# Kernel optimization log

Measured on AMD Instinct MI355X. Metric: run time of the kernel, lower is better.

The kernel has to match this reference:

```python
import jax, jax.numpy as jnp
import numpy as np

DIM, CTX_DIM, HEADS, HIDDEN = 1024, 768, 16, 4096
HEAD_DIM = DIM // HEADS
SCALE = HEAD_DIM ** -0.5


def _layernorm(x, w, b, eps=1e-5):
    mu = jnp.mean(x, axis=-1, keepdims=True)
    var = jnp.var(x, axis=-1, keepdims=True)
    return (x - mu) * jax.lax.rsqrt(var + eps) * w + b


def _heads(t):  # [B, L, H*D] -> [B, H, L, D]
    B, L, _ = t.shape
    return t.reshape(B, L, HEADS, HEAD_DIM).transpose(0, 2, 1, 3)


def _merge(t):  # [B, H, L, D] -> [B, L, H*D]
    B, H, L, D = t.shape
    return t.transpose(0, 2, 1, 3).reshape(B, L, H * D)


def _attn(xq, xkv, qw, qb, kw, kb, vw, vb, pw, pb):
    q = _heads(xq @ qw.T + qb)
    k = _heads(xkv @ kw.T + kb)
    v = _heads(xkv @ vw.T + vb)
    scores = jnp.einsum('bhld,bhsd->bhls', q, k) * SCALE
    probs = jax.nn.softmax(scores, axis=-1)
    out = _merge(jnp.einsum('bhls,bhsd->bhld', probs, v))
    return out @ pw.T + pb


def setup_inputs() -> dict:
    key = jax.random.key(0)
    ks = jax.random.split(key, 16)
    s = 0.02
    d = {
        'x': jax.random.normal(ks[0], (4, 2048, DIM), jnp.float32),
        'context': jax.random.normal(ks[1], (4, 77, CTX_DIM), jnp.float32),
        'ln1_w': jnp.ones((DIM,)), 'ln1_b': jnp.zeros((DIM,)),
        'ln2_w': jnp.ones((DIM,)), 'ln2_b': jnp.zeros((DIM,)),
        'ln3_w': jnp.ones((DIM,)), 'ln3_b': jnp.zeros((DIM,)),
        'sa_qw': jax.random.normal(ks[2], (DIM, DIM)) * s, 'sa_qb': jnp.zeros((DIM,)),
        'sa_kw': jax.random.normal(ks[3], (DIM, DIM)) * s, 'sa_kb': jnp.zeros((DIM,)),
        'sa_vw': jax.random.normal(ks[4], (DIM, DIM)) * s, 'sa_vb': jnp.zeros((DIM,)),
        'sa_pw': jax.random.normal(ks[5], (DIM, DIM)) * s, 'sa_pb': jnp.zeros((DIM,)),
        'ca_qw': jax.random.normal(ks[6], (DIM, DIM)) * s, 'ca_qb': jnp.zeros((DIM,)),
        'ca_kw': jax.random.normal(ks[7], (DIM, CTX_DIM)) * s, 'ca_kb': jnp.zeros((DIM,)),
        'ca_vw': jax.random.normal(ks[8], (DIM, CTX_DIM)) * s, 'ca_vb': jnp.zeros((DIM,)),
        'ca_pw': jax.random.normal(ks[9], (DIM, DIM)) * s, 'ca_pb': jnp.zeros((DIM,)),
        'fc1_w': jax.random.normal(ks[10], (HIDDEN, DIM)) * s, 'fc1_b': jnp.zeros((HIDDEN,)),
        'fc2_w': jax.random.normal(ks[11], (DIM, HIDDEN)) * s, 'fc2_b': jnp.zeros((DIM,)),
    }
    return d


def reference(x, context, ln1_w, ln1_b, ln2_w, ln2_b, ln3_w, ln3_b,
              sa_qw, sa_qb, sa_kw, sa_kb, sa_vw, sa_vb, sa_pw, sa_pb,
              ca_qw, ca_qb, ca_kw, ca_kb, ca_vw, ca_vb, ca_pw, ca_pb,
              fc1_w, fc1_b, fc2_w, fc2_b):
    h = _layernorm(x, ln1_w, ln1_b)
    x = x + _attn(h, h, sa_qw, sa_qb, sa_kw, sa_kb, sa_vw, sa_vb, sa_pw, sa_pb)
    h = _layernorm(x, ln2_w, ln2_b)
    x = x + _attn(h, context, ca_qw, ca_qb, ca_kw, ca_kb, ca_vw, ca_vb, ca_pw, ca_pb)
    h = _layernorm(x, ln3_w, ln3_b)
    h = jax.nn.gelu(h @ fc1_w.T + fc1_b, approximate=False)  # torch nn.GELU = exact
    x = x + (h @ fc2_w.T + fc2_b)
    return x
```

## Files before the change

### kernel.cpp

```cpp
#include <hip/hip_runtime.h>
#include <hip/hip_bf16.h>
#include <cstdint>
#include <cstddef>

typedef __attribute__((ext_vector_type(8))) short bf16x8;
typedef __attribute__((ext_vector_type(4))) float f32x4;
typedef __attribute__((ext_vector_type(16))) float f32x16;

__device__ __forceinline__ unsigned short f2bf(float f) {
  union { float f; unsigned u; } c; c.f = f;
  unsigned r = c.u + 0x7FFFu + ((c.u >> 16) & 1u);
  return (unsigned short)(r >> 16);
}

__device__ __forceinline__ unsigned cvtpk(float lo, float hi) {
  unsigned r;
  asm("v_cvt_pk_bf16_f32 %0, %1, %2" : "=v"(r) : "v"(lo), "v"(hi));
  return r;
}

__device__ __forceinline__ int xcd_swz(int bid, int nwg) {
  const int cpx = nwg >> 3;
  return (bid & 7) * cpx + (bid >> 3);
}

typedef const __attribute__((address_space(1))) unsigned int* gas_ptr;
typedef __attribute__((address_space(3))) unsigned int* las_ptr;

__device__ __forceinline__ void gload16(const unsigned short* g, unsigned short* l) {
  __builtin_amdgcn_global_load_lds((gas_ptr)g, (las_ptr)l, 16, 0, 0);
}

struct WJ { const float* s; unsigned short* d; int nblk; };
struct WJobs { WJ j[10]; };

__global__ void wconv_k(WJobs jb) {
  const int bid = blockIdx.x;
  int base = 0, ji = -1;
  #pragma unroll
  for (int k = 0; k < 10; ++k) {
    const int nb = jb.j[k].nblk;
    if (ji < 0) { if (bid < base + nb) ji = k; else base += nb; }
  }
  const int i = (bid - base) * 256 + threadIdx.x;
  float4 v = ((const float4*)jb.j[ji].s)[i];
  ushort4 o;
  o.x = f2bf(v.x); o.y = f2bf(v.y); o.z = f2bf(v.z); o.w = f2bf(v.w);
  ((ushort4*)jb.j[ji].d)[i] = o;
}

__global__ void ctxpad_k(const float* __restrict__ ctx, unsigned short* __restrict__ out) {
  int i = blockIdx.x * blockDim.x + threadIdx.x;
  if (i >= 512 * 192) return;
  int r = i / 192, c4 = i % 192;
  int b = r >> 7, s = r & 127;
  ushort4 o = {0, 0, 0, 0};
  if (s < 77) {
    float4 v = ((const float4*)(ctx + (size_t)(b * 77 + s) * 768))[c4];
    o.x = f2bf(v.x); o.y = f2bf(v.y); o.z = f2bf(v.z); o.w = f2bf(v.w);
  }
  ((ushort4*)out)[i] = o;
}

__global__ __launch_bounds__(256)
void ln_k(const float* __restrict__ x, const float* __restrict__ w,
          const float* __restrict__ b, unsigned short* __restrict__ out) {
  int row = blockIdx.x, tid = threadIdx.x;
  float4 v = ((const float4*)(x + (size_t)row * 1024))[tid];
  float s = v.x + v.y + v.z + v.w;
  float s2 = v.x * v.x + v.y * v.y + v.z * v.z + v.w * v.w;
  #pragma unroll
  for (int m = 1; m < 64; m <<= 1) { s += __shfl_xor(s, m); s2 += __shfl_xor(s2, m); }
  __shared__ float ps[4], ps2[4];
  int wv = tid >> 6;
  if ((tid & 63) == 0) { ps[wv] = s; ps2[wv] = s2; }
  __syncthreads();
  s = ps[0] + ps[1] + ps[2] + ps[3];
  s2 = ps2[0] + ps2[1] + ps2[2] + ps2[3];
  float mu = s * (1.0f / 1024.0f);
  float var = s2 * (1.0f / 1024.0f) - mu * mu;
  float rstd = rsqrtf(var + 1e-5f);
  float4 wv4 = ((const float4*)w)[tid];
  float4 bv4 = ((const float4*)b)[tid];
  ushort4 o;
  o.x = f2bf((v.x - mu) * rstd * wv4.x + bv4.x);
  o.y = f2bf((v.y - mu) * rstd * wv4.y + bv4.y);
  o.z = f2bf((v.z - mu) * rstd * wv4.z + bv4.z);
  o.w = f2bf((v.w - mu) * rstd * wv4.w + bv4.w);
  ((ushort4*)(out + (size_t)row * 1024))[tid] = o;
}

#define SG_A(BUF, H, TE)                                                       \
  _Pragma("unroll")                                                            \
  for (int j = 0; j < AHL; ++j)                                                \
    __builtin_amdgcn_global_load_lds(                                          \
        (gas_ptr)(gA + (TE) + (size_t)((H) * (BM / 2) + j * 64) * (size_t)K),  \
        (las_ptr)(lds_all + (BUF) * AELEMS +                                   \
                  (((H) * (BM / 2) + j * 64) + w * 8) * 64),                   \
        16, 0, 0);

#define SG_B(BUF, H, TE)                                                       \
  _Pragma("unroll")                                                            \
  for (int j = 0; j < BHL; ++j)                                                \
    __builtin_amdgcn_global_load_lds(                                          \
        (gas_ptr)(gB + (TE) + (size_t)((H) * (BN / 2) + j * 64) * (size_t)K),  \
        (las_ptr)(lds_all + 2 * AELEMS + (BUF) * BELEMS +                      \
                  (((H) * (BN / 2) + j * 64) + w * 8) * 64),                   \
        16, 0, 0);

#define RD_A(MHh, BUF)                                                         \
  _Pragma("unroll")                                                            \
  for (int i = 0; i < MH; ++i) {                                               \
    const int r = ((MHh) * MH + i) * 32 + wr * 16 + ln;                        \
    _Pragma("unroll")                                                          \
    for (int kc = 0; kc < 2; ++kc)                                             \
      af[i][kc] = *(const bf16x8*)((const char*)lds_all + (BUF) * ABYTES +     \
                    r * 128 + (((kc * 4 + lg) ^ (r & 7)) * 16));               \
  }

#define RD_B(NHh, BUF)                                                         \
  _Pragma("unroll")                                                            \
  for (int i = 0; i < NIH; ++i) {                                              \
    const int ni = (NHh) * NIH + i;                                            \
    const int r = ni * 64 + wcc * 16 + ln;                                     \
    _Pragma("unroll")                                                          \
    for (int kc = 0; kc < 2; ++kc)                                             \
      bfr[ni][kc] = *(const bf16x8*)((const char*)lds_all + 2 * ABYTES +       \
                    (BUF) * BBYTES + r * 128 + (((kc * 4 + lg) ^ (r & 7)) * 16)); \
  }

#define QUAD(MHh, NHh)                                                         \
  __builtin_amdgcn_s_setprio(1);                                               \
  _Pragma("unroll")                                                            \
  for (int kc = 0; kc < 2; ++kc)                                               \
    _Pragma("unroll")                                                          \
    for (int i = 0; i < MH; ++i)                                               \
      _Pragma("unroll")                                                        \
      for (int j2 = 0; j2 < NIH; ++j2) {                                       \
        const int mi = (MHh) * MH + i, ni = (NHh) * NIH + j2;                  \
        if constexpr (SWAP)                                                    \
          acc[mi][ni] = __builtin_amdgcn_mfma_f32_16x16x32_bf16(               \
              bfr[ni][kc], af[i][kc], acc[mi][ni], 0, 0, 0);                   \
        else                                                                   \
          acc[mi][ni] = __builtin_amdgcn_mfma_f32_16x16x32_bf16(               \
              af[i][kc], bfr[ni][kc], acc[mi][ni], 0, 0, 0);                   \
      }                                                                        \
  __builtin_amdgcn_s_setprio(0);

#define VM_TILE()                                                              \
  do { if constexpr (BM == 256) asm volatile("s_waitcnt vmcnt(6)" ::: "memory"); \
       else                     asm volatile("s_waitcnt vmcnt(3)" ::: "memory"); } while (0)

#define TILE(BUF, TE)                                                          \
  {                                                                            \
    const int t = t2 + ((TE) / 64);                                            \
                       \
    RD_A(0, BUF) RD_B(0, BUF)                                                  \
    if (t + 1 < NT) { SG_B((BUF) ^ 1, 1, (TE) + 64) }                          \
    __builtin_amdgcn_s_barrier();                                              \
    asm volatile("s_waitcnt lgkmcnt(0)" ::: "memory");                         \
    __builtin_amdgcn_sched_barrier(0);                                         \
    QUAD(0, 0)                                                                 \
    __builtin_amdgcn_s_barrier();                                              \
                    \
    RD_B(1, BUF)                                                               \
    if (t + 2 < NT) { SG_A(BUF, 0, (TE) + 128) }                               \
    __builtin_amdgcn_s_barrier();                                              \
    asm volatile("s_waitcnt lgkmcnt(0)" ::: "memory");                         \
    __builtin_amdgcn_sched_barrier(0);                                         \
    QUAD(0, 1)                                                                 \
    __builtin_amdgcn_s_barrier();                                              \
                    \
    RD_A(1, BUF)                                                               \
    if (t + 2 < NT) { SG_B(BUF, 0, (TE) + 128) }                               \
    __builtin_amdgcn_s_barrier();                                              \
    asm volatile("s_waitcnt lgkmcnt(0)" ::: "memory");                         \
    __builtin_amdgcn_sched_barrier(0);                                         \
    QUAD(1, 0)                                                                 \
    __builtin_amdgcn_s_barrier();                                              \
     \
    if (t + 2 < NT) { SG_A(BUF, 1, (TE) + 128) }                               \
    __builtin_amdgcn_s_barrier();                                              \
    __builtin_amdgcn_sched_barrier(0);                                         \
    QUAD(1, 1)                                                                 \
    if (t + 2 < NT) { VM_TILE(); }                                             \
    else            { asm volatile("s_waitcnt vmcnt(0)" ::: "memory"); }       \
    __builtin_amdgcn_s_barrier();                                              \
  }

template<int BM, int BN, int EPI, int SWAP, int MINW>
__global__ __launch_bounds__(512, MINW)
void gemm8(const unsigned short* __restrict__ A, const unsigned short* __restrict__ Bw,
           const float* __restrict__ bias0, const float* __restrict__ bias1,
           const float* __restrict__ res, void* __restrict__ C0, void* __restrict__ C1,
           int M, int N, int K, float scale0, int nsplit, int vtL) {
  (void)M;
  constexpr int MI = BM / 32;
  constexpr int MH = MI / 2;
  constexpr int AHL = BM / 128;
  constexpr int NI = BN / 64;
  constexpr int NIH = NI / 2;
  constexpr int BHL = BN / 128;
  constexpr int AELEMS = BM * 64;
  constexpr int BELEMS = BN * 64;
  constexpr int ABYTES = AELEMS * 2;
  constexpr int BBYTES = BELEMS * 2;
  __shared__ unsigned short lds_all[2 * AELEMS + 2 * BELEMS];

  const int tid = threadIdx.x;
  const int w = tid >> 6, lane = tid & 63;
  const int wr = w >> 2, wcc = w & 3;
  const int ln = lane & 15, lg = lane >> 4;
  const int nbn = N / BN;
  const int bid = xcd_swz(blockIdx.x, gridDim.x);
  const int bm = bid / nbn, bn = bid % nbn;
  const int NT = K >> 6;

  const int crow = tid >> 3;
  const int cslot = (tid & 7) ^ (crow & 7);

  const unsigned short* gA = A + ((size_t)(bm * BM) + crow) * K + cslot * 8;
  const unsigned short* gB = Bw + ((size_t)(bn * BN) + crow) * K + cslot * 8;

  bf16x8 af[MH][2], bfr[NI][2];
  f32x4 acc[MI][NI] = {};

  SG_A(0, 0, 0) SG_B(0, 0, 0) SG_B(0, 1, 0) SG_A(0, 1, 0)
  if (NT > 1) { SG_A(1, 0, 64) SG_B(1, 0, 64) SG_A(1, 1, 64) }
  VM_TILE();
  __builtin_amdgcn_s_barrier();

  for (int t2 = 0; t2 < NT; t2 += 2) {
    TILE(0, 0)
    TILE(1, 64)
    gA += 128; gB += 128;
  }

  const int rowbase = bm * BM + wr * 16;
  const int colbase = bn * BN + wcc * 16;
  if constexpr (EPI == 1) {
    #pragma unroll
    for (int ni = 0; ni < NI; ++ni) {
      const int col = colbase + ni * 64 + ln;
      const float bv = bias0[col];
      const int hh = col >> 6, dd = col & 63;
      #pragma unroll
      for (int mi = 0; mi < MI; ++mi) {
        const int row0 = rowbase + mi * 32 + lg * 4;
        const int bb = row0 / vtL, ss = row0 % vtL;
        ushort4 pk;
        pk.x = f2bf(acc[mi][ni][0] + bv);
        pk.y = f2bf(acc[mi][ni][1] + bv);
        pk.z = f2bf(acc[mi][ni][2] + bv);
        pk.w = f2bf(acc[mi][ni][3] + bv);
        *(ushort4*)((unsigned short*)C0 + ((size_t)((bb * 16 + hh) * 64 + dd)) * vtL + ss) = pk;
      }
    }
  } else {
    #pragma unroll
    for (int ni = 0; ni < NI; ++ni) {
      const int n0 = colbase + ni * 64 + lg * 4;
      const bool lo = (n0 < nsplit);
      const float* bp = lo ? bias0 : bias1;
      const float sc = lo ? scale0 : 1.0f;
      const int nc = lo ? n0 : n0 - nsplit;
      const int ldc = lo ? nsplit : N - nsplit;
      void* Cp = lo ? C0 : C1;
      const float4 b4 = *(const float4*)(bp + nc);
      #pragma unroll
      for (int mi = 0; mi < MI; ++mi) {
        const size_t mrow = (size_t)rowbase + mi * 32 + ln;
        float v0 = acc[mi][ni][0] + b4.x;
        float v1 = acc[mi][ni][1] + b4.y;
        float v2 = acc[mi][ni][2] + b4.z;
        float v3 = acc[mi][ni][3] + b4.w;
        if constexpr (EPI == 0) {
          ushort4 pk;
          pk.x = f2bf(v0 * sc); pk.y = f2bf(v1 * sc);
          pk.z = f2bf(v2 * sc); pk.w = f2bf(v3 * sc);
          *(ushort4*)((unsigned short*)Cp + mrow * ldc + nc) = pk;
        } else if constexpr (EPI == 2) {
          const float4 r4 = *(const float4*)(res + mrow * ldc + nc);
          float4 o4 = { v0 + r4.x, v1 + r4.y, v2 + r4.z, v3 + r4.w };
          *(float4*)((float*)Cp + mrow * ldc + nc) = o4;
        } else {
          v0 = 0.5f * v0 * (1.0f + erff(v0 * 0.70710678118654752f));
          v1 = 0.5f * v1 * (1.0f + erff(v1 * 0.70710678118654752f));
          v2 = 0.5f * v2 * (1.0f + erff(v2 * 0.70710678118654752f));
          v3 = 0.5f * v3 * (1.0f + erff(v3 * 0.70710678118654752f));
          ushort4 pk;
          pk.x = f2bf(v0); pk.y = f2bf(v1); pk.z = f2bf(v2); pk.w = f2bf(v3);
          *(ushort4*)((unsigned short*)Cp + mrow * ldc + nc) = pk;
        }
      }
    }
  }
}

__global__ __launch_bounds__(256, 4)
void flash_k(const unsigned short* __restrict__ Q, const unsigned short* __restrict__ Kg,
             const unsigned short* __restrict__ VT, unsigned short* __restrict__ O,
             int Lq, int Lkpad, int kvlen) {
  const int qblocks = Lq >> 7;
  const int bid = xcd_swz(blockIdx.x, gridDim.x);
  const int bh = bid / qblocks, qb = bid - bh * qblocks;
  const int b = bh >> 4, h = bh & 15;
  const int tid = threadIdx.x, w = tid >> 6, lane = tid & 63;
  const int l31 = lane & 31, hi = lane >> 5;

  __shared__ unsigned short Ks[2][64 * 64];
  __shared__ unsigned short Vs[2][64 * 64];

  const size_t qrow = (size_t)b * Lq + qb * 128 + w * 32 + l31;
  bf16x8 qf[4];
  #pragma unroll
  for (int ds = 0; ds < 4; ++ds)
    qf[ds] = *(const bf16x8*)(Q + qrow * 1024 + h * 64 + ds * 16 + hi * 8);

  f32x16 oacc[2] = {};
  f32x4 lacc = {};

  const int nst = (kvlen + 63) >> 6;
  const int srow = lane >> 3;
  const int gslot = (lane & 7) ^ srow;

  auto STAGE = [&](int buf, int st) {
    #pragma unroll
    for (int i = 0; i < 2; ++i) {
      const int r = i * 32 + w * 8 + srow;
      gload16(Kg + ((size_t)b * Lkpad + st * 64 + r) * 1024 + h * 64 + gslot * 8,
              &Ks[buf][(i * 32 + w * 8) * 64]);
      gload16(VT + ((size_t)bh * 64 + r) * Lkpad + (size_t)st * 64 + gslot * 8,
              &Vs[buf][(i * 32 + w * 8) * 64]);
    }
  };

  STAGE(0, 0);

  for (int st = 0; st < nst; ++st) {
    const int cur = st & 1;
    __syncthreads();
    if (st + 1 < nst) STAGE(cur ^ 1, st + 1);

    const char* Kb = (const char*)Ks[cur];
    const char* Vb = (const char*)Vs[cur];

    #pragma unroll
    for (int kb = 0; kb < 2; ++kb) {
      f32x16 s = {};
      {
        const int r = kb * 32 + l31;
        const int sw = (r & 7) << 4;
        __builtin_amdgcn_s_setprio(1);
        #pragma unroll
        for (int ds = 0; ds < 4; ++ds) {
          bf16x8 kf = *(const bf16x8*)(Kb + r * 128 + ((ds * 32 + hi * 16) ^ sw));
          s = __builtin_amdgcn_mfma_f32_32x32x16_bf16(kf, qf[ds], s, 0, 0, 0);
        }
        __builtin_amdgcn_s_setprio(0);
      }

      if (st * 64 + 64 > kvlen) {
        const int kbase = st * 64 + kb * 32 + hi * 4;
        #pragma unroll
        for (int r = 0; r < 16; ++r)
          if (kbase + (r & 3) + 8 * (r >> 2) >= kvlen) s[r] = -1e30f;
      }

      #pragma unroll
      for (int r = 0; r < 16; ++r) s[r] = __builtin_amdgcn_exp2f(s[r]);
      #pragma unroll
      for (int rq = 0; rq < 4; ++rq) {
        f32x4 t = { s[rq * 4 + 0], s[rq * 4 + 1], s[rq * 4 + 2], s[rq * 4 + 3] };
        lacc += t;
      }

      bf16x8 pf[2];
      #pragma unroll
      for (int m = 0; m < 2; ++m) {
        unsigned u0 = cvtpk(s[8 * m + 0], s[8 * m + 1]);
        unsigned u1 = cvtpk(s[8 * m + 2], s[8 * m + 3]);
        unsigned u2 = cvtpk(s[8 * m + 4], s[8 * m + 5]);
        unsigned u3 = cvtpk(s[8 * m + 6], s[8 * m + 7]);
        asm volatile("v_permlane32_swap_b32 %0, %1" : "+v"(u0), "+v"(u2));
        asm volatile("v_permlane32_swap_b32 %0, %1" : "+v"(u1), "+v"(u3));
        union { unsigned u[4]; bf16x8 v; } fr;
        fr.u[0] = u0; fr.u[1] = u1; fr.u[2] = u2; fr.u[3] = u3;
        pf[m] = fr.v;
      }

      {
        const int sw2 = (l31 & 7) << 4;
        __builtin_amdgcn_s_setprio(1);
        #pragma unroll
        for (int db = 0; db < 2; ++db) {
          const int r = db * 32 + l31;
          #pragma unroll
          for (int m = 0; m < 2; ++m) {
            bf16x8 vf = *(const bf16x8*)(Vb + r * 128 +
                          ((kb * 64 + m * 32 + hi * 16) ^ sw2));
            oacc[db] = __builtin_amdgcn_mfma_f32_32x32x16_bf16(vf, pf[m], oacc[db], 0, 0, 0);
          }
        }
        __builtin_amdgcn_s_setprio(0);
      }
    }
  }

  float lt = lacc[0] + lacc[1] + lacc[2] + lacc[3];
  lt += __shfl_xor(lt, 32);
  const float inv = 1.0f / lt;
  #pragma unroll
  for (int db = 0; db < 2; ++db)
    #pragma unroll
    for (int rg = 0; rg < 4; ++rg) {
      ushort4 pk;
      pk.x = f2bf(oacc[db][rg * 4 + 0] * inv);
      pk.y = f2bf(oacc[db][rg * 4 + 1] * inv);
      pk.z = f2bf(oacc[db][rg * 4 + 2] * inv);
      pk.w = f2bf(oacc[db][rg * 4 + 3] * inv);
      *(ushort4*)(O + qrow * 1024 + h * 64 + db * 32 + rg * 8 + hi * 4) = pk;
    }
}

extern "C" void kernel_launch(void* const* d_in, const int* in_sizes, int n_in,
                              void* d_out, int out_size, void* d_ws, size_t ws_size,
                              hipStream_t stream) {
  (void)in_sizes; (void)n_in; (void)out_size; (void)ws_size;
  const float* x     = (const float*)d_in[0];
  const float* ctx   = (const float*)d_in[1];
  const float* ln1_w = (const float*)d_in[2];
  const float* ln1_b = (const float*)d_in[3];
  const float* ln2_w = (const float*)d_in[4];
  const float* ln2_b = (const float*)d_in[5];
  const float* ln3_w = (const float*)d_in[6];
  const float* ln3_b = (const float*)d_in[7];
  const float* sa_qw = (const float*)d_in[8];  const float* sa_qb = (const float*)d_in[9];
  const float* sa_kw = (const float*)d_in[10]; const float* sa_kb = (const float*)d_in[11];
  const float* sa_vw = (const float*)d_in[12]; const float* sa_vb = (const float*)d_in[13];
  const float* sa_pw = (const float*)d_in[14]; const float* sa_pb = (const float*)d_in[15];
  const float* ca_qw = (const float*)d_in[16]; const float* ca_qb = (const float*)d_in[17];
  const float* ca_kw = (const float*)d_in[18]; const float* ca_kb = (const float*)d_in[19];
  const float* ca_vw = (const float*)d_in[20]; const float* ca_vb = (const float*)d_in[21];
  const float* ca_pw = (const float*)d_in[22]; const float* ca_pb = (const float*)d_in[23];
  const float* fc1_w = (const float*)d_in[24]; const float* fc1_b = (const float*)d_in[25];
  const float* fc2_w = (const float*)d_in[26]; const float* fc2_b = (const float*)d_in[27];

  char* ws = (char*)d_ws;
  size_t o = 0;
  auto give = [&](size_t bytes) { size_t r = o; o += (bytes + 255) & ~(size_t)255; return r; };
  const size_t SQ = 1048576, SC = 786432, SF = 4194304;
  unsigned short* w_qk  = (unsigned short*)(ws + give(2 * SQ * 2));
  unsigned short* w_v   = (unsigned short*)(ws + give(SQ * 2));
  unsigned short* w_p   = (unsigned short*)(ws + give(SQ * 2));
  unsigned short* w_caq = (unsigned short*)(ws + give(SQ * 2));
  unsigned short* w_cak = (unsigned short*)(ws + give(SC * 2));
  unsigned short* w_cav = (unsigned short*)(ws + give(SC * 2));
  unsigned short* w_cap = (unsigned short*)(ws + give(SQ * 2));
  unsigned short* w_f1  = (unsigned short*)(ws + give(SF * 2));
  unsigned short* w_f2  = (unsigned short*)(ws + give(SF * 2));
  unsigned short* ctxb  = (unsigned short*)(ws + give(512 * 768 * 2));
  unsigned short* hbuf  = (unsigned short*)(ws + give(8192 * 1024 * 2));
  unsigned short* qbuf  = (unsigned short*)(ws + give(8192 * 1024 * 2));
  unsigned short* kbuf  = (unsigned short*)(ws + give(8192 * 1024 * 2));
  unsigned short* vtbuf = (unsigned short*)(ws + give(8192 * 1024 * 2));
  unsigned short* obuf  = (unsigned short*)(ws + give(8192 * 1024 * 2));
  float*          xc    = (float*)(ws + give(8192 * 1024 * 4));
  unsigned short* gbuf  = qbuf;

  const float QSCALE = 0.125f * 1.44269504088896341f;

  WJobs jb;
  jb.j[0] = { sa_qw, w_qk,      (int)(SQ / 1024) };
  jb.j[1] = { sa_kw, w_qk + SQ, (int)(SQ / 1024) };
  jb.j[2] = { sa_vw, w_v,       (int)(SQ / 1024) };
  jb.j[3] = { sa_pw, w_p,       (int)(SQ / 1024) };
  jb.j[4] = { ca_qw, w_caq,     (int)(SQ / 1024) };
  jb.j[5] = { ca_kw, w_cak,     (int)(SC / 1024) };
  jb.j[6] = { ca_vw, w_cav,     (int)(SC / 1024) };
  jb.j[7] = { ca_pw, w_cap,     (int)(SQ / 1024) };
  jb.j[8] = { fc1_w, w_f1,      (int)(SF / 1024) };
  jb.j[9] = { fc2_w, w_f2,      (int)(SF / 1024) };
  int totblk = 0;
  for (int k = 0; k < 10; ++k) totblk += jb.j[k].nblk;

  wconv_k<<<totblk, 256, 0, stream>>>(jb);
  ctxpad_k<<<384, 256, 0, stream>>>(ctx, ctxb);

  ln_k<<<8192, 256, 0, stream>>>(x, ln1_w, ln1_b, hbuf);
  gemm8<256, 256, 0, 1, 2><<<256, 512, 0, stream>>>(hbuf, w_qk, sa_qb, sa_kb, nullptr, qbuf, kbuf,
                                                    8192, 2048, 1024, QSCALE, 1024, 0);
  gemm8<128, 128, 1, 0, 4><<<512, 512, 0, stream>>>(hbuf, w_v, sa_vb, nullptr, nullptr, vtbuf, nullptr,
                                                    8192, 1024, 1024, 1.0f, 1024, 2048);
  flash_k<<<1024, 256, 0, stream>>>(qbuf, kbuf, vtbuf, obuf, 2048, 2048, 2048);
  gemm8<128, 128, 2, 1, 4><<<512, 512, 0, stream>>>(obuf, w_p, sa_pb, nullptr, x, xc, nullptr,
                                                    8192, 1024, 1024, 1.0f, 1024, 0);

  ln_k<<<8192, 256, 0, stream>>>(xc, ln2_w, ln2_b, hbuf);
  gemm8<128, 128, 0, 1, 4><<<512, 512, 0, stream>>>(hbuf, w_caq, ca_qb, nullptr, nullptr, qbuf, nullptr,
                                                    8192, 1024, 1024, QSCALE, 1024, 0);
  gemm8<128, 128, 0, 1, 4><<<32, 512, 0, stream>>>(ctxb, w_cak, ca_kb, nullptr, nullptr, kbuf, nullptr,
                                                   512, 1024, 768, 1.0f, 1024, 0);
  gemm8<128, 128, 1, 0, 4><<<32, 512, 0, stream>>>(ctxb, w_cav, ca_vb, nullptr, nullptr, vtbuf, nullptr,
                                                   512, 1024, 768, 1.0f, 1024, 128);
  flash_k<<<1024, 256, 0, stream>>>(qbuf, kbuf, vtbuf, obuf, 2048, 128, 77);
  gemm8<128, 128, 2, 1, 4><<<512, 512, 0, stream>>>(obuf, w_cap, ca_pb, nullptr, xc, xc, nullptr,
                                                    8192, 1024, 1024, 1.0f, 1024, 0);

  ln_k<<<8192, 256, 0, stream>>>(xc, ln3_w, ln3_b, hbuf);
  gemm8<256, 256, 3, 1, 2><<<512, 512, 0, stream>>>(hbuf, w_f1, fc1_b, nullptr, nullptr, gbuf, nullptr,
                                                    8192, 4096, 1024, 1.0f, 4096, 0);
  gemm8<128, 128, 2, 1, 4><<<512, 512, 0, stream>>>(gbuf, w_f2, fc2_b, nullptr, xc, d_out, nullptr,
                                                    8192, 1024, 4096, 1.0f, 1024, 0);
}
```

Baseline: 482.1 us.

## Software-pipeline LDS fragment reads across GEMM quads and tiles

Restructures the per-tile schedule of the bf16 MFMA GEMM so LDS fragment reads for the next quadrant (and the next tile's first A/B fragments) are issued before the current quadrant's MFMAs, using a double-buffered A fragment register array. It removes several s_barriers per tile and relaxes the vmcnt wait in the steady state, aiming to hide LDS latency behind MFMA work. This costs more VGPRs for the second A fragment set and depends on subtle ordering of global_load_lds writes against reads, which risks races or register spills.

```diff
diff --git a/kernel.cpp b/kernel.cpp
--- a/kernel.cpp
+++ b/kernel.cpp
@@ -114,7 +114,7 @@
     const int r = ((MHh) * MH + i) * 32 + wr * 16 + ln;                        \
     _Pragma("unroll")                                                          \
     for (int kc = 0; kc < 2; ++kc)                                             \
-      af[i][kc] = *(const bf16x8*)((const char*)lds_all + (BUF) * ABYTES +     \
+      af[MHh][i][kc] = *(const bf16x8*)((const char*)lds_all + (BUF) * ABYTES +\
                     r * 128 + (((kc * 4 + lg) ^ (r & 7)) * 16));               \
   }
 
@@ -140,51 +140,53 @@
         const int mi = (MHh) * MH + i, ni = (NHh) * NIH + j2;                  \
         if constexpr (SWAP)                                                    \
           acc[mi][ni] = __builtin_amdgcn_mfma_f32_16x16x32_bf16(               \
-              bfr[ni][kc], af[i][kc], acc[mi][ni], 0, 0, 0);                   \
+              bfr[ni][kc], af[MHh][i][kc], acc[mi][ni], 0, 0, 0);              \
         else                                                                   \
           acc[mi][ni] = __builtin_amdgcn_mfma_f32_16x16x32_bf16(               \
-              af[i][kc], bfr[ni][kc], acc[mi][ni], 0, 0, 0);                   \
+              af[MHh][i][kc], bfr[ni][kc], acc[mi][ni], 0, 0, 0);              \
       }                                                                        \
   __builtin_amdgcn_s_setprio(0);
 
 #define VM_TILE()                                                              \
+  do { if constexpr (BM == 256) asm volatile("s_waitcnt vmcnt(4)" ::: "memory"); \
+       else                     asm volatile("s_waitcnt vmcnt(2)" ::: "memory"); } while (0)
+
+#define VM_PRO()                                                               \
   do { if constexpr (BM == 256) asm volatile("s_waitcnt vmcnt(6)" ::: "memory"); \
        else                     asm volatile("s_waitcnt vmcnt(3)" ::: "memory"); } while (0)
+
+#define LGK0()                                                                 \
+  asm volatile("s_waitcnt lgkmcnt(0)" ::: "memory");                           \
+  __builtin_amdgcn_sched_barrier(0);
 
 #define TILE(BUF, TE)                                                          \
   {                                                                            \
     const int t = t2 + ((TE) / 64);                                            \
-                       \
-    RD_A(0, BUF) RD_B(0, BUF)                                                  \
+                 \
     if (t + 1 < NT) { SG_B((BUF) ^ 1, 1, (TE) + 64) }                          \
-    __builtin_amdgcn_s_barrier();                                              \
-    asm volatile("s_waitcnt lgkmcnt(0)" ::: "memory");                         \
-    __builtin_amdgcn_sched_barrier(0);                                         \
+    LGK0()                                                                     \
+    RD_B(1, BUF)                                                               \
     QUAD(0, 0)                                                                 \
     __builtin_amdgcn_s_barrier();                                              \
-                    \
-    RD_B(1, BUF)                                                               \
+                  \
     if (t + 2 < NT) { SG_A(BUF, 0, (TE) + 128) }                               \
-    __builtin_amdgcn_s_barrier();                                              \
-    asm volatile("s_waitcnt lgkmcnt(0)" ::: "memory");                         \
-    __builtin_amdgcn_sched_barrier(0);                                         \
+    LGK0()                                                                     \
+    RD_A(1, BUF)                                                               \
     QUAD(0, 1)                                                                 \
     __builtin_amdgcn_s_barrier();                                              \
-                    \
-    RD_A(1, BUF)                                                               \
+       \
     if (t + 2 < NT) { SG_B(BUF, 0, (TE) + 128) }                               \
-    __builtin_amdgcn_s_barrier();                                              \
-    asm volatile("s_waitcnt lgkmcnt(0)" ::: "memory");                         \
-    __builtin_amdgcn_sched_barrier(0);                                         \
-    QUAD(1, 0)                                                                 \
-    __builtin_amdgcn_s_barrier();                                              \
-     \
-    if (t + 2 < NT) { SG_A(BUF, 1, (TE) + 128) }                               \
-    __builtin_amdgcn_s_barrier();                                              \
-    __builtin_amdgcn_sched_barrier(0);                                         \
+    LGK0()                                                                     \
     QUAD(1, 1)                                                                 \
     if (t + 2 < NT) { VM_TILE(); }                                             \
     else            { asm volatile("s_waitcnt vmcnt(0)" ::: "memory"); }       \
+    __builtin_amdgcn_s_barrier();                                              \
+    __builtin_amdgcn_sched_barrier(0);                                         \
+                                                            \
+    if (t + 1 < NT) { RD_A(0, (BUF) ^ 1) }                                     \
+    QUAD(1, 0)                                                                 \
+    if (t + 1 < NT) { RD_B(0, (BUF) ^ 1) }                                     \
+    if (t + 2 < NT) { SG_A(BUF, 1, (TE) + 128) }                               \
     __builtin_amdgcn_s_barrier();                                              \
   }
 
@@ -222,13 +224,15 @@
   const unsigned short* gA = A + ((size_t)(bm * BM) + crow) * K + cslot * 8;
   const unsigned short* gB = Bw + ((size_t)(bn * BN) + crow) * K + cslot * 8;
 
-  bf16x8 af[MH][2], bfr[NI][2];
+  bf16x8 af[2][MH][2], bfr[NI][2];
   f32x4 acc[MI][NI] = {};
 
   SG_A(0, 0, 0) SG_B(0, 0, 0) SG_B(0, 1, 0) SG_A(0, 1, 0)
   if (NT > 1) { SG_A(1, 0, 64) SG_B(1, 0, 64) SG_A(1, 1, 64) }
-  VM_TILE();
+  VM_PRO();
   __builtin_amdgcn_s_barrier();
+  __builtin_amdgcn_sched_barrier(0);
+  RD_A(0, 0) RD_B(0, 0)
 
   for (int t2 = 0; t2 < NT; t2 += 2) {
     TILE(0, 0)
```

Result: slower. 560.7 us (+16.3%).
